# Performance work log

Measured on AMD Instinct MI355X. Metric: run time of the kernel, lower is better.

Reference implementation:

```python
import jax, jax.numpy as jnp
import numpy as np

NUM_HEADS = 16
THETA = 10000.0


def _apply_rope(x, pos):
    # x: [b, h, t, d_k], pos: [t] int
    d = x.shape[-1]
    inv_freq = THETA ** (-jnp.arange(0, d, 2, dtype=jnp.float32) / d)  # [d/2]
    ang = pos.astype(jnp.float32)[:, None] * inv_freq                  # [t, d/2]
    cos, sin = jnp.cos(ang), jnp.sin(ang)
    x1, x2 = x[..., ::2], x[..., 1::2]
    r1 = x1 * cos - x2 * sin
    r2 = x1 * sin + x2 * cos
    return jnp.stack([r1, r2], axis=-1).reshape(x.shape)


def setup_inputs() -> dict:
    key = jax.random.key(0)
    k1, k2, k3 = jax.random.split(key, 3)
    b, t, dm = 4, 2048, 2048
    in_features = jax.random.normal(k1, (b, t, dm), dtype=jnp.float32)
    token_positions = jnp.arange(t, dtype=jnp.int64)
    W_qkv = jax.random.normal(k2, (3 * dm, dm), dtype=jnp.float32) * 0.02
    W_o = jax.random.normal(k3, (dm, dm), dtype=jnp.float32) * 0.02
    return {"in_features": in_features, "token_positions": token_positions,
            "W_qkv": W_qkv, "W_o": W_o}


def reference(in_features, token_positions, W_qkv, W_o):
    b, t, dm = in_features.shape
    h = NUM_HEADS
    dk = dm // h
    # fused QKV projection (Linear: y = x W^T)
    qkv = in_features @ W_qkv.T                       # [b, t, 3*dm]
    q, k, v = jnp.split(qkv, 3, axis=-1)
    def to_heads(x):
        return x.reshape(b, t, h, dk).transpose(0, 2, 1, 3)  # [b, h, t, dk]
    q, k, v = to_heads(q), to_heads(k), to_heads(v)
    q = _apply_rope(q, token_positions)
    k = _apply_rope(k, token_positions)
    # causal SDPA
    scale = 1.0 / np.sqrt(dk).astype(np.float32)
    scores = jnp.einsum('bhqd,bhkd->bhqk', q, k) * scale
    causal = jnp.tril(jnp.ones((t, t), dtype=bool))
    scores = jnp.where(causal, scores, jnp.finfo(scores.dtype).min)
    attn = jax.nn.softmax(scores, axis=-1)
    out = jnp.einsum('bhqk,bhkd->bhqd', attn, v)      # [b, h, t, dk]
    out = out.transpose(0, 2, 1, 3).reshape(b, t, dm)
    return out @ W_o.T
```

## Files before the change

kernel.cpp:

```cpp
#include <hip/hip_runtime.h>

typedef unsigned short u16;
typedef __attribute__((ext_vector_type(8))) short s8v;
typedef __attribute__((ext_vector_type(8))) __bf16 bf8;
typedef __attribute__((ext_vector_type(4))) float f4v;

#define GLB(p) ((const __attribute__((address_space(1))) void*)(p))
#define LDS(p) ((__attribute__((address_space(3))) void*)(p))

static __device__ __forceinline__ float b2f(u16 u) {
    union { unsigned int i; float f; } v; v.i = ((unsigned int)u) << 16; return v.f;
}
static __device__ __forceinline__ u16 f2b(float f) {
    union { float f; unsigned int i; } v; v.f = f;
    v.i += 0x7fffu + ((v.i >> 16) & 1u);
    return (u16)(v.i >> 16);
}

__global__ __launch_bounds__(256) void k_conv(const float* __restrict__ in,
                                              u16* __restrict__ out, int n4) {
    int i = blockIdx.x * 256 + threadIdx.x;
    if (i >= n4) return;
    float4 v = ((const float4*)in)[i];
    union { u16 u[4]; unsigned long long ll; } o;
    o.u[0] = f2b(v.x); o.u[1] = f2b(v.y); o.u[2] = f2b(v.z); o.u[3] = f2b(v.w);
    ((unsigned long long*)out)[i] = o.ll;
}

template<int MODE>
__global__ __launch_bounds__(512, 2) void k_gemm_bt(
    const u16* __restrict__ A, const u16* __restrict__ B,
    int K, int N, int gx,
    u16* __restrict__ Qb, u16* __restrict__ Kb, u16* __restrict__ Vt,
    float* __restrict__ Cf)
{
    extern __shared__ __align__(16) u16 Ls[];

    const int t    = threadIdx.x;
    const int lane = t & 63;
    const int wid  = t >> 6;
    const int wm = wid >> 2, wn = wid & 3;
    const int la = lane & 15, lb = lane >> 4;

    const int bid = (int)blockIdx.x;
    const int id2 = (bid & 7) * ((int)gridDim.x >> 3) + (bid >> 3);
    const int bx = id2 % gx, by = id2 / gx;
    const long arow0 = (long)by * 256;
    const long brow0 = (long)bx * 256;

    const int sr = t >> 3;
    const int sg = (t & 7) ^ (sr & 7);
    const u16* Asrc = A + (arow0 + sr) * (long)K + sg * 8;
    const u16* Bsrc = B + (brow0 + sr) * (long)K + sg * 8;
    const long K64 = 64 * (long)K, K128 = 128 * (long)K;
    u16* ldst = Ls + t * 8;

#define STG(q_, op_, h_, kt_) do {                                              \
        const u16* s_ = ((op_) ? Bsrc : Asrc) + (h_) * K128 + (long)(kt_) * 64; \
        u16* d_ = ldst + (q_) * 32768 + (op_) * 16384 + (h_) * 8192;            \
        __builtin_amdgcn_global_load_lds(GLB(s_),       LDS(d_),        16, 0, 0); \
        __builtin_amdgcn_global_load_lds(GLB(s_ + K64), LDS(d_ + 4096), 16, 0, 0); \
    } while (0)
#define RD(off) (*(const bf8*)(Ls + (off)))

    f4v acc[8][4];
#pragma unroll
    for (int m = 0; m < 8; m++)
#pragma unroll
        for (int n = 0; n < 4; n++) acc[m][n] = (f4v){0.f, 0.f, 0.f, 0.f};

    const int r7 = la & 7;
    const int gA0 = (lb ^ r7) * 8;
    const int gA1 = ((lb ^ r7) ^ 4) * 8;
    const int aRow = wm * 8192 + la * 64;
    const int bRow = 16384 + (wn >> 1) * 8192 + ((wn & 1) * 64 + la) * 64;

    const int NKT = K >> 6;
    STG(0, 0, 0, 0); STG(0, 0, 1, 0); STG(0, 1, 0, 0); STG(0, 1, 1, 0);
    asm volatile("s_waitcnt vmcnt(0)" ::: "memory");
    __builtin_amdgcn_s_barrier();

    for (int X = 0; X < NKT; ++X) {
        const int D = (X & 1) << 15;
        const int q = (X + 1) & 1;
        const int S = (X + 1 < NKT) ? X + 1 : NKT - 1;
        bf8 aR[4][2], b0[2][2], b1[2][2];

#pragma unroll
        for (int mi = 0; mi < 4; mi++) {
            aR[mi][0] = RD(D + aRow + mi * 1024 + gA0);
            aR[mi][1] = RD(D + aRow + mi * 1024 + gA1);
        }
#pragma unroll
        for (int nl = 0; nl < 2; nl++) {
            b0[nl][0] = RD(D + bRow + nl * 1024 + gA0);
            b0[nl][1] = RD(D + bRow + nl * 1024 + gA1);
        }
        STG(q, 0, 0, S); STG(q, 0, 1, S); STG(q, 1, 0, S); STG(q, 1, 1, S);
        __builtin_amdgcn_s_barrier();
        __builtin_amdgcn_s_setprio(1);
#pragma unroll
        for (int mi = 0; mi < 4; mi++)
#pragma unroll
            for (int nl = 0; nl < 2; nl++) {
                acc[mi][nl] = __builtin_amdgcn_mfma_f32_16x16x32_bf16(aR[mi][0], b0[nl][0], acc[mi][nl], 0, 0, 0);
                acc[mi][nl] = __builtin_amdgcn_mfma_f32_16x16x32_bf16(aR[mi][1], b0[nl][1], acc[mi][nl], 0, 0, 0);
            }
        __builtin_amdgcn_s_setprio(0);

#pragma unroll
        for (int nl = 0; nl < 2; nl++) {
            b1[nl][0] = RD(D + bRow + (2 + nl) * 1024 + gA0);
            b1[nl][1] = RD(D + bRow + (2 + nl) * 1024 + gA1);
        }
        __builtin_amdgcn_s_barrier();
        __builtin_amdgcn_s_setprio(1);
#pragma unroll
        for (int mi = 0; mi < 4; mi++)
#pragma unroll
            for (int nl = 0; nl < 2; nl++) {
                acc[mi][2 + nl] = __builtin_amdgcn_mfma_f32_16x16x32_bf16(aR[mi][0], b1[nl][0], acc[mi][2 + nl], 0, 0, 0);
                acc[mi][2 + nl] = __builtin_amdgcn_mfma_f32_16x16x32_bf16(aR[mi][1], b1[nl][1], acc[mi][2 + nl], 0, 0, 0);
            }
        __builtin_amdgcn_s_setprio(0);

#pragma unroll
        for (int mi = 0; mi < 4; mi++) {
            aR[mi][0] = RD(D + aRow + (4 + mi) * 1024 + gA0);
            aR[mi][1] = RD(D + aRow + (4 + mi) * 1024 + gA1);
        }
        __builtin_amdgcn_s_barrier();
        __builtin_amdgcn_s_setprio(1);
#pragma unroll
        for (int mi = 0; mi < 4; mi++)
#pragma unroll
            for (int nl = 0; nl < 2; nl++) {
                acc[4 + mi][2 + nl] = __builtin_amdgcn_mfma_f32_16x16x32_bf16(aR[mi][0], b1[nl][0], acc[4 + mi][2 + nl], 0, 0, 0);
                acc[4 + mi][2 + nl] = __builtin_amdgcn_mfma_f32_16x16x32_bf16(aR[mi][1], b1[nl][1], acc[4 + mi][2 + nl], 0, 0, 0);
            }
        __builtin_amdgcn_s_setprio(0);

        asm volatile("s_waitcnt vmcnt(0)" ::: "memory");
        __builtin_amdgcn_s_barrier();
        __builtin_amdgcn_s_setprio(1);
#pragma unroll
        for (int mi = 0; mi < 4; mi++)
#pragma unroll
            for (int nl = 0; nl < 2; nl++) {
                acc[4 + mi][nl] = __builtin_amdgcn_mfma_f32_16x16x32_bf16(aR[mi][0], b0[nl][0], acc[4 + mi][nl], 0, 0, 0);
                acc[4 + mi][nl] = __builtin_amdgcn_mfma_f32_16x16x32_bf16(aR[mi][1], b0[nl][1], acc[4 + mi][nl], 0, 0, 0);
            }
        __builtin_amdgcn_s_setprio(0);
    }
#undef STG
#undef RD

    if (MODE == 1) {
#pragma unroll
        for (int mi = 0; mi < 8; mi++)
#pragma unroll
            for (int ni = 0; ni < 4; ni++) {
                const long grow0 = arow0 + wm * 128 + mi * 16 + lb * 4;
                const int  gcol  = (int)brow0 + wn * 64 + ni * 16 + la;
#pragma unroll
                for (int i = 0; i < 4; i++)
                    Cf[(grow0 + i) * (long)N + gcol] = acc[mi][ni][i];
            }
        return;
    }

    __syncthreads();
    const int part = (int)(brow0 >> 11);
    const int colp = (int)brow0 & 2047;
    const int h0   = colp >> 7;
    const int bidx = (int)(arow0 >> 11);
    const int t0   = (int)arow0 & 2047;

    if (part == 2) {
#pragma unroll
        for (int mi = 0; mi < 8; mi++)
#pragma unroll
            for (int ni = 0; ni < 4; ni++) {
                const int tlb = wm * 128 + mi * 16 + lb * 4;
                const int dl  = wn * 64 + ni * 16 + la;
#pragma unroll
                for (int i2 = 0; i2 < 2; i2++) {
                    unsigned int pk = (unsigned int)f2b(acc[mi][ni][i2 * 2])
                                    | ((unsigned int)f2b(acc[mi][ni][i2 * 2 + 1]) << 16);
                    *(unsigned int*)(Ls + dl * 264 + tlb + i2 * 2) = pk;
                }
            }
        __syncthreads();
        const int w = wid;
#pragma unroll
        for (int j = 0; j < 16; j++) {
            const int dl = j * 16 + w * 2 + (lane >> 5);
            const int c  = lane & 31;
            bf8 v = *(const bf8*)(Ls + dl * 264 + c * 8);
            const long bh = (long)(bidx * 16 + h0 + (dl >> 7));
            *(bf8*)(Vt + (bh << 18) + ((long)(dl & 127) << 11) + t0 + c * 8) = v;
        }
    } else {
        u16* dst = (part == 0) ? Qb : Kb;
#pragma unroll
        for (int mi = 0; mi < 8; mi++)
#pragma unroll
            for (int ni = 0; ni < 4; ni++) {
                const int tlb = wm * 128 + mi * 16 + lb * 4;
                const int dl  = wn * 64 + ni * 16 + la;
#pragma unroll
                for (int i = 0; i < 4; i++)
                    Ls[(tlb + i) * 264 + dl] = f2b(acc[mi][ni][i]);
            }
        __syncthreads();
#pragma unroll
        for (int j = 0; j < 16; j++) {
            const int R  = j * 32 + (t >> 4);
            const int tl = R >> 1, hh = R & 1, c = t & 15;
            bf8 v = *(const bf8*)(Ls + tl * 264 + hh * 128 + c * 8);
            const long bh = (long)(bidx * 16 + h0 + hh);
            *(bf8*)(dst + ((bh << 11) + t0 + tl) * 128 + c * 8) = v;
        }
    }
}

__global__ __launch_bounds__(256) void k_rope(u16* __restrict__ Qb, u16* __restrict__ Kb,
                                              const int* __restrict__ pos) {
    const int idx = blockIdx.x * 256 + threadIdx.x;
    const int j  = idx & 63;
    const int t  = (idx >> 6) & 2047;
    const int bh = (idx >> 17) & 63;
    u16* P = (idx >> 23) ? Kb : Qb;
    const long off = ((((long)bh << 11) + t) << 7) + 2 * j;
    unsigned int raw = *(unsigned int*)(P + off);
    float x1 = b2f((u16)(raw & 0xffffu));
    float x2 = b2f((u16)(raw >> 16));
    float invf = exp2f((float)j * -0.20762050593046014f);
    float ang = (float)pos[t] * invf;
    float sn, cs;
    sincosf(ang, &sn, &cs);
    unsigned int o = (unsigned int)f2b(x1 * cs - x2 * sn)
                   | ((unsigned int)f2b(x1 * sn + x2 * cs) << 16);
    *(unsigned int*)(P + off) = o;
}

__global__ __launch_bounds__(512) void k_attn(const u16* __restrict__ Qb,
                                              const u16* __restrict__ Kb,
                                              const u16* __restrict__ Vt,
                                              u16* __restrict__ Ob)
{
    __shared__ __align__(16) u16 Ks[2][32 * 128];
    __shared__ __align__(16) u16 Vs[2][64 * 64];
    __shared__ __align__(16) u16 Pl[8][32 * 32];

    const int tid  = threadIdx.x;
    const int lane = tid & 63;
    const int w    = tid >> 6;
    const int la = lane & 15, lb = lane >> 4;
    const int qg = 7 - ((int)blockIdx.x >> 6);
    const int bh = blockIdx.x & 63;
    const long base = (long)bh << 18;
    const int qt = qg * 8 + w;
    const int q0 = qt * 32;
    const int tiles_w = qt + 1;
    const int NT = qg * 8 + 8;
    const float scale = 0.08838834764831845f;

    bf8 qf[2][4];
#pragma unroll
    for (int m = 0; m < 2; m++)
#pragma unroll
        for (int kb = 0; kb < 4; kb++)
            qf[m][kb] = *(const bf8*)(Qb + base + (long)(q0 + m * 16 + la) * 128 + kb * 32 + lb * 8);

    f4v o[2][8];
#pragma unroll
    for (int m = 0; m < 2; m++)
#pragma unroll
        for (int n = 0; n < 8; n++) o[m][n] = (f4v){0.f, 0.f, 0.f, 0.f};
    float lst[2][4];
#pragma unroll
    for (int m = 0; m < 2; m++)
#pragma unroll
        for (int i = 0; i < 4; i++) lst[m][i] = 0.f;

    char* Pb = (char*)(Pl[w]);

    const int ko = tid * 16;
    const int kr = ko >> 8, kc = (ko & 255) ^ ((kr & 7) << 4);
    const int vo = tid * 16;
    const int vR = vo >> 7, vc = (vo & 127) ^ ((vR & 7) << 4);
    const int vd = 2 * vR + (vc >> 6), vt = (vc & 63) >> 1;

#define STAGE(buf, jt_) do {                                                        \
        const int kv0_ = (jt_) * 32;                                               \
        __builtin_amdgcn_global_load_lds(                                          \
            GLB(Kb + base + (long)(kv0_ + kr) * 128 + (kc >> 1)),                  \
            LDS((u16*)Ks[buf] + tid * 8), 16, 0, 0);                               \
        __builtin_amdgcn_global_load_lds(                                          \
            GLB(Vt + base + ((long)vd << 11) + kv0_ + vt),                         \
            LDS((u16*)Vs[buf] + tid * 8), 16, 0, 0);                               \
    } while (0)

    STAGE(0, 0);

    for (int jt = 0; jt < NT; ++jt) {
        const int buf = jt & 1;
        __syncthreads();
        if (jt + 1 < NT) STAGE(buf ^ 1, jt + 1);

        if (jt < tiles_w) {
            const char* KsB = (const char*)Ks[buf];
            const char* VsB = (const char*)Vs[buf];

            f4v s[2][2];
            s[0][0] = s[0][1] = s[1][0] = s[1][1] = (f4v){0.f, 0.f, 0.f, 0.f};
#pragma unroll
            for (int n = 0; n < 2; n++) {
                const int row = n * 16 + la;
#pragma unroll
                for (int kb = 0; kb < 4; kb++) {
                    bf8 kf = *(const bf8*)(KsB + row * 256 + ((kb * 64 + lb * 16) ^ ((row & 7) << 4)));
                    s[0][n] = __builtin_amdgcn_mfma_f32_16x16x32_bf16(qf[0][kb], kf, s[0][n], 0, 0, 0);
                    s[1][n] = __builtin_amdgcn_mfma_f32_16x16x32_bf16(qf[1][kb], kf, s[1][n], 0, 0, 0);
                }
            }

            bf8 vf[8];
#pragma unroll
            for (int nO = 0; nO < 8; nO++) {
                const int R = nO * 8 + (la >> 1);
                vf[nO] = *(const bf8*)(VsB + R * 128 + (((la & 1) * 64 + lb * 16) ^ ((R & 7) << 4)));
            }

            const bool diag = (jt == qt);
            float p[2][2][4];
#pragma unroll
            for (int m = 0; m < 2; m++)
#pragma unroll
                for (int n = 0; n < 2; n++)
#pragma unroll
                    for (int i = 0; i < 4; i++) {
                        float v = __expf(fmaf(s[m][n][i], scale, -8.0f));
                        if (diag && (n * 16 + la) > (m * 16 + lb * 4 + i)) v = 0.f;
                        p[m][n][i] = v;
                        lst[m][i] += v;
                    }

#pragma unroll
            for (int m = 0; m < 2; m++)
#pragma unroll
                for (int n = 0; n < 2; n++)
#pragma unroll
                    for (int i = 0; i < 4; i++) {
                        const int row = m * 16 + lb * 4 + i;
                        const int colb = (n * 16 + la) * 2;
                        *(u16*)(Pb + row * 64 + (colb ^ ((row & 3) << 4))) = f2b(p[m][n][i]);
                    }
            bf8 pa[2];
#pragma unroll
            for (int am = 0; am < 2; am++) {
                const int row = am * 16 + la;
                pa[am] = *(const bf8*)(Pb + row * 64 + ((lb * 16) ^ ((row & 3) << 4)));
            }
#pragma unroll
            for (int nO = 0; nO < 8; nO++) {
                o[0][nO] = __builtin_amdgcn_mfma_f32_16x16x32_bf16(pa[0], vf[nO], o[0][nO], 0, 0, 0);
                o[1][nO] = __builtin_amdgcn_mfma_f32_16x16x32_bf16(pa[1], vf[nO], o[1][nO], 0, 0, 0);
            }
        }
        __syncthreads();
    }
#undef STAGE

    float linv[2][4];
#pragma unroll
    for (int m = 0; m < 2; m++)
#pragma unroll
        for (int i = 0; i < 4; i++) {
            float l = lst[m][i];
            l += __shfl_xor(l, 1);
            l += __shfl_xor(l, 2);
            l += __shfl_xor(l, 4);
            l += __shfl_xor(l, 8);
            linv[m][i] = 1.0f / l;
        }

    const int b = bh >> 4, h = bh & 15;
#pragma unroll
    for (int m = 0; m < 2; m++)
#pragma unroll
        for (int nO = 0; nO < 8; nO++)
#pragma unroll
            for (int i = 0; i < 4; i++) {
                const int row = q0 + m * 16 + lb * 4 + i;
                const int d = nO * 16 + la;
                Ob[((long)(b * 2048 + row) << 11) + h * 128 + d] = f2b(o[m][nO][i] * linv[m][i]);
            }
}

extern "C" void kernel_launch(void* const* d_in, const int* in_sizes, int n_in,
                              void* d_out, int out_size, void* d_ws, size_t ws_size,
                              hipStream_t stream)
{
    const float* X    = (const float*)d_in[0];
    const int*   pos  = (const int*)d_in[1];
    const float* Wqkv = (const float*)d_in[2];
    const float* Wo   = (const float*)d_in[3];
    float* out = (float*)d_out;

    char* ws = (char*)d_ws;
    u16* Xb    = (u16*)(ws + 0);
    u16* Wqkvb = (u16*)(ws + 33554432);
    u16* Wob   = (u16*)(ws + 58720256);
    u16* Qb    = (u16*)(ws + 67108864);
    u16* Kb    = (u16*)(ws + 100663296);
    u16* Vt    = (u16*)(ws + 134217728);
    u16* Ob    = (u16*)(ws + 167772160);

    k_conv<<<16384, 256, 0, stream>>>(X, Xb, 4194304);
    k_conv<<<12288, 256, 0, stream>>>(Wqkv, Wqkvb, 3145728);
    k_conv<<<4096, 256, 0, stream>>>(Wo, Wob, 1048576);
    k_gemm_bt<0><<<768, 512, 139392, stream>>>(Xb, Wqkvb, 2048, 6144, 24, Qb, Kb, Vt, nullptr);
    k_rope<<<65536, 256, 0, stream>>>(Qb, Kb, pos);
    k_attn<<<512, 512, 0, stream>>>(Qb, Kb, Vt, Ob);
    k_gemm_bt<1><<<256, 512, 139392, stream>>>(Ob, Wob, 2048, 2048, 8, nullptr, nullptr, nullptr, out);
}
```

Before: 436.2 us.

## Fuse RoPE into QKV GEMM epilogue, merge conversions, triple-buffer GEMM k-loop

Three separate changes. The three fp32-to-bf16 conversion launches become one launch that picks its source by index. RoPE moves into the Q/K store epilogue of the QKV GEMM, using fast __sincosf, so the standalone rope pass that re-read and re-wrote Q and K is gone. The GEMM main loop switches from a 64-wide double-buffered k-tile with four barriers per step to a 32-wide triple-buffered tile with one barrier per step, keeping more loads in flight. The risks are lower sincos accuracy at large angles and a different LDS bank pattern from the new 4-way swizzle.

```diff
diff --git a/kernel.cpp b/kernel.cpp
--- a/kernel.cpp
+++ b/kernel.cpp
@@ -17,14 +17,21 @@
     return (u16)(v.i >> 16);
 }
 
-__global__ __launch_bounds__(256) void k_conv(const float* __restrict__ in,
-                                              u16* __restrict__ out, int n4) {
+__global__ __launch_bounds__(256) void k_conv(const float* __restrict__ X,
+                                              const float* __restrict__ Wq,
+                                              const float* __restrict__ Wo,
+                                              u16* __restrict__ Xb,
+                                              u16* __restrict__ Wqb,
+                                              u16* __restrict__ Wob) {
     int i = blockIdx.x * 256 + threadIdx.x;
-    if (i >= n4) return;
-    float4 v = ((const float4*)in)[i];
+    const float* in; u16* out; int off;
+    if (i < 4194304)      { in = X;  out = Xb;  off = i; }
+    else if (i < 7340032) { in = Wq; out = Wqb; off = i - 4194304; }
+    else                  { in = Wo; out = Wob; off = i - 7340032; }
+    float4 v = ((const float4*)in)[off];
     union { u16 u[4]; unsigned long long ll; } o;
     o.u[0] = f2b(v.x); o.u[1] = f2b(v.y); o.u[2] = f2b(v.z); o.u[3] = f2b(v.w);
-    ((unsigned long long*)out)[i] = o.ll;
+    ((unsigned long long*)out)[off] = o.ll;
 }
 
 template<int MODE>
@@ -32,7 +39,7 @@
     const u16* __restrict__ A, const u16* __restrict__ B,
     int K, int N, int gx,
     u16* __restrict__ Qb, u16* __restrict__ Kb, u16* __restrict__ Vt,
-    float* __restrict__ Cf)
+    float* __restrict__ Cf, const int* __restrict__ pos)
 {
     extern __shared__ __align__(16) u16 Ls[];
 
@@ -48,18 +55,20 @@
     const long arow0 = (long)by * 256;
     const long brow0 = (long)bx * 256;
 
-    const int sr = t >> 3;
-    const int sg = (t & 7) ^ (sr & 7);
+    const int sr = t >> 2;
+    const int sg = (t & 3) ^ (sr & 3);
     const u16* Asrc = A + (arow0 + sr) * (long)K + sg * 8;
     const u16* Bsrc = B + (brow0 + sr) * (long)K + sg * 8;
-    const long K64 = 64 * (long)K, K128 = 128 * (long)K;
+    const long K128 = 128 * (long)K;
     u16* ldst = Ls + t * 8;
 
-#define STG(q_, op_, h_, kt_) do {                                              \
-        const u16* s_ = ((op_) ? Bsrc : Asrc) + (h_) * K128 + (long)(kt_) * 64; \
-        u16* d_ = ldst + (q_) * 32768 + (op_) * 16384 + (h_) * 8192;            \
-        __builtin_amdgcn_global_load_lds(GLB(s_),       LDS(d_),        16, 0, 0); \
-        __builtin_amdgcn_global_load_lds(GLB(s_ + K64), LDS(d_ + 4096), 16, 0, 0); \
+#define STG(q_, kt_) do {                                                          \
+        const long ko_ = (long)(kt_) * 32;                                         \
+        u16* d_ = ldst + (q_) * 16384;                                             \
+        __builtin_amdgcn_global_load_lds(GLB(Asrc + ko_),         LDS(d_),         16, 0, 0); \
+        __builtin_amdgcn_global_load_lds(GLB(Asrc + K128 + ko_),  LDS(d_ + 4096),  16, 0, 0); \
+        __builtin_amdgcn_global_load_lds(GLB(Bsrc + ko_),         LDS(d_ + 8192),  16, 0, 0); \
+        __builtin_amdgcn_global_load_lds(GLB(Bsrc + K128 + ko_),  LDS(d_ + 12288), 16, 0, 0); \
     } while (0)
 #define RD(off) (*(const bf8*)(Ls + (off)))
 
@@ -69,89 +78,38 @@
 #pragma unroll
         for (int n = 0; n < 4; n++) acc[m][n] = (f4v){0.f, 0.f, 0.f, 0.f};
 
-    const int r7 = la & 7;
-    const int gA0 = (lb ^ r7) * 8;
-    const int gA1 = ((lb ^ r7) ^ 4) * 8;
-    const int aRow = wm * 8192 + la * 64;
-    const int bRow = 16384 + (wn >> 1) * 8192 + ((wn & 1) * 64 + la) * 64;
-
-    const int NKT = K >> 6;
-    STG(0, 0, 0, 0); STG(0, 0, 1, 0); STG(0, 1, 0, 0); STG(0, 1, 1, 0);
+    const int gA = (lb ^ (la & 3)) * 8;
+    const int aBase = wm * 4096 + la * 32 + gA;
+    const int bBase = 8192 + (wn >> 1) * 4096 + ((wn & 1) * 64 + la) * 32 + gA;
+
+    const int NKT = K >> 5;
+    STG(0, 0); STG(1, 1);
+    asm volatile("s_waitcnt vmcnt(4)" ::: "memory");
+    __builtin_amdgcn_s_barrier();
+
+    for (int X = 0; X < NKT; ++X) {
+        const int D = (X % 3) * 16384;
+        int S = X + 2; if (S > NKT - 1) S = NKT - 1;
+        STG((X + 2) % 3, S);
+
+        bf8 aF[8], bF[4];
+#pragma unroll
+        for (int mi = 0; mi < 8; mi++) aF[mi] = RD(D + aBase + mi * 512);
+#pragma unroll
+        for (int ni = 0; ni < 4; ni++) bF[ni] = RD(D + bBase + ni * 512);
+
+        __builtin_amdgcn_s_setprio(1);
+#pragma unroll
+        for (int mi = 0; mi < 8; mi++)
+#pragma unroll
+            for (int ni = 0; ni < 4; ni++)
+                acc[mi][ni] = __builtin_amdgcn_mfma_f32_16x16x32_bf16(aF[mi], bF[ni], acc[mi][ni], 0, 0, 0);
+        __builtin_amdgcn_s_setprio(0);
+
+        asm volatile("s_waitcnt vmcnt(4)" ::: "memory");
+        __builtin_amdgcn_s_barrier();
+    }
     asm volatile("s_waitcnt vmcnt(0)" ::: "memory");
-    __builtin_amdgcn_s_barrier();
-
-    for (int X = 0; X < NKT; ++X) {
-        const int D = (X & 1) << 15;
-        const int q = (X + 1) & 1;
-        const int S = (X + 1 < NKT) ? X + 1 : NKT - 1;
-        bf8 aR[4][2], b0[2][2], b1[2][2];
-
-#pragma unroll
-        for (int mi = 0; mi < 4; mi++) {
-            aR[mi][0] = RD(D + aRow + mi * 1024 + gA0);
-            aR[mi][1] = RD(D + aRow + mi * 1024 + gA1);
-        }
-#pragma unroll
-        for (int nl = 0; nl < 2; nl++) {
-            b0[nl][0] = RD(D + bRow + nl * 1024 + gA0);
-            b0[nl][1] = RD(D + bRow + nl * 1024 + gA1);
-        }
-        STG(q, 0, 0, S); STG(q, 0, 1, S); STG(q, 1, 0, S); STG(q, 1, 1, S);
-        __builtin_amdgcn_s_barrier();
-        __builtin_amdgcn_s_setprio(1);
-#pragma unroll
-        for (int mi = 0; mi < 4; mi++)
-#pragma unroll
-            for (int nl = 0; nl < 2; nl++) {
-                acc[mi][nl] = __builtin_amdgcn_mfma_f32_16x16x32_bf16(aR[mi][0], b0[nl][0], acc[mi][nl], 0, 0, 0);
-                acc[mi][nl] = __builtin_amdgcn_mfma_f32_16x16x32_bf16(aR[mi][1], b0[nl][1], acc[mi][nl], 0, 0, 0);
-            }
-        __builtin_amdgcn_s_setprio(0);
-
-#pragma unroll
-        for (int nl = 0; nl < 2; nl++) {
-            b1[nl][0] = RD(D + bRow + (2 + nl) * 1024 + gA0);
-            b1[nl][1] = RD(D + bRow + (2 + nl) * 1024 + gA1);
-        }
-        __builtin_amdgcn_s_barrier();
-        __builtin_amdgcn_s_setprio(1);
-#pragma unroll
-        for (int mi = 0; mi < 4; mi++)
-#pragma unroll
-            for (int nl = 0; nl < 2; nl++) {
-                acc[mi][2 + nl] = __builtin_amdgcn_mfma_f32_16x16x32_bf16(aR[mi][0], b1[nl][0], acc[mi][2 + nl], 0, 0, 0);
-                acc[mi][2 + nl] = __builtin_amdgcn_mfma_f32_16x16x32_bf16(aR[mi][1], b1[nl][1], acc[mi][2 + nl], 0, 0, 0);
-            }
-        __builtin_amdgcn_s_setprio(0);
-
-#pragma unroll
-        for (int mi = 0; mi < 4; mi++) {
-            aR[mi][0] = RD(D + aRow + (4 + mi) * 1024 + gA0);
-            aR[mi][1] = RD(D + aRow + (4 + mi) * 1024 + gA1);
-        }
-        __builtin_amdgcn_s_barrier();
-        __builtin_amdgcn_s_setprio(1);
-#pragma unroll
-        for (int mi = 0; mi < 4; mi++)
-#pragma unroll
-            for (int nl = 0; nl < 2; nl++) {
-                acc[4 + mi][2 + nl] = __builtin_amdgcn_mfma_f32_16x16x32_bf16(aR[mi][0], b1[nl][0], acc[4 + mi][2 + nl], 0, 0, 0);
-                acc[4 + mi][2 + nl] = __builtin_amdgcn_mfma_f32_16x16x32_bf16(aR[mi][1], b1[nl][1], acc[4 + mi][2 + nl], 0, 0, 0);
-            }
-        __builtin_amdgcn_s_setprio(0);
-
-        asm volatile("s_waitcnt vmcnt(0)" ::: "memory");
-        __builtin_amdgcn_s_barrier();
-        __builtin_amdgcn_s_setprio(1);
-#pragma unroll
-        for (int mi = 0; mi < 4; mi++)
-#pragma unroll
-            for (int nl = 0; nl < 2; nl++) {
-                acc[4 + mi][nl] = __builtin_amdgcn_mfma_f32_16x16x32_bf16(aR[mi][0], b0[nl][0], acc[4 + mi][nl], 0, 0, 0);
-                acc[4 + mi][nl] = __builtin_amdgcn_mfma_f32_16x16x32_bf16(aR[mi][1], b0[nl][1], acc[4 + mi][nl], 0, 0, 0);
-            }
-        __builtin_amdgcn_s_setprio(0);
-    }
 #undef STG
 #undef RD
 
@@ -191,10 +149,9 @@
                 }
             }
         __syncthreads();
-        const int w = wid;
 #pragma unroll
         for (int j = 0; j < 16; j++) {
-            const int dl = j * 16 + w * 2 + (lane >> 5);
+            const int dl = j * 16 + wid * 2 + (lane >> 5);
             const int c  = lane & 31;
             bf8 v = *(const bf8*)(Ls + dl * 264 + c * 8);
             const long bh = (long)(bidx * 16 + h0 + (dl >> 7));
@@ -213,35 +170,31 @@
                     Ls[(tlb + i) * 264 + dl] = f2b(acc[mi][ni][i]);
             }
         __syncthreads();
+        const int c = t & 15;
+        float invf[4];
+#pragma unroll
+        for (int p2 = 0; p2 < 4; p2++)
+            invf[p2] = exp2f((float)(c * 4 + p2) * -0.20762050593046014f);
 #pragma unroll
         for (int j = 0; j < 16; j++) {
             const int R  = j * 32 + (t >> 4);
-            const int tl = R >> 1, hh = R & 1, c = t & 15;
-            bf8 v = *(const bf8*)(Ls + tl * 264 + hh * 128 + c * 8);
+            const int tl = R >> 1, hh = R & 1;
+            s8v v = *(const s8v*)(Ls + tl * 264 + hh * 128 + c * 8);
+            const float pf = (float)pos[t0 + tl];
+            union { u16 u[8]; s8v v; } ov;
+#pragma unroll
+            for (int p2 = 0; p2 < 4; p2++) {
+                float x1 = b2f((u16)v[2 * p2]);
+                float x2 = b2f((u16)v[2 * p2 + 1]);
+                float sn, cs;
+                __sincosf(pf * invf[p2], &sn, &cs);
+                ov.u[2 * p2]     = f2b(x1 * cs - x2 * sn);
+                ov.u[2 * p2 + 1] = f2b(x1 * sn + x2 * cs);
+            }
             const long bh = (long)(bidx * 16 + h0 + hh);
-            *(bf8*)(dst + ((bh << 11) + t0 + tl) * 128 + c * 8) = v;
+            *(s8v*)(dst + ((bh << 11) + t0 + tl) * 128 + c * 8) = ov.v;
         }
     }
-}
-
-__global__ __launch_bounds__(256) void k_rope(u16* __restrict__ Qb, u16* __restrict__ Kb,
-                                              const int* __restrict__ pos) {
-    const int idx = blockIdx.x * 256 + threadIdx.x;
-    const int j  = idx & 63;
-    const int t  = (idx >> 6) & 2047;
-    const int bh = (idx >> 17) & 63;
-    u16* P = (idx >> 23) ? Kb : Qb;
-    const long off = ((((long)bh << 11) + t) << 7) + 2 * j;
-    unsigned int raw = *(unsigned int*)(P + off);
-    float x1 = b2f((u16)(raw & 0xffffu));
-    float x2 = b2f((u16)(raw >> 16));
-    float invf = exp2f((float)j * -0.20762050593046014f);
-    float ang = (float)pos[t] * invf;
-    float sn, cs;
-    sincosf(ang, &sn, &cs);
-    unsigned int o = (unsigned int)f2b(x1 * cs - x2 * sn)
-                   | ((unsigned int)f2b(x1 * sn + x2 * cs) << 16);
-    *(unsigned int*)(P + off) = o;
 }
 
 __global__ __launch_bounds__(512) void k_attn(const u16* __restrict__ Qb,
@@ -418,11 +371,8 @@
     u16* Vt    = (u16*)(ws + 134217728);
     u16* Ob    = (u16*)(ws + 167772160);
 
-    k_conv<<<16384, 256, 0, stream>>>(X, Xb, 4194304);
-    k_conv<<<12288, 256, 0, stream>>>(Wqkv, Wqkvb, 3145728);
-    k_conv<<<4096, 256, 0, stream>>>(Wo, Wob, 1048576);
-    k_gemm_bt<0><<<768, 512, 139392, stream>>>(Xb, Wqkvb, 2048, 6144, 24, Qb, Kb, Vt, nullptr);
-    k_rope<<<65536, 256, 0, stream>>>(Qb, Kb, pos);
+    k_conv<<<32768, 256, 0, stream>>>(X, Wqkv, Wo, Xb, Wqkvb, Wob);
+    k_gemm_bt<0><<<768, 512, 135168, stream>>>(Xb, Wqkvb, 2048, 6144, 24, Qb, Kb, Vt, nullptr, pos);
     k_attn<<<512, 512, 0, stream>>>(Qb, Kb, Vt, Ob);
-    k_gemm_bt<1><<<256, 512, 139392, stream>>>(Ob, Wob, 2048, 2048, 8, nullptr, nullptr, nullptr, out);
-}
+    k_gemm_bt<1><<<256, 512, 98304, stream>>>(Ob, Wob, 2048, 2048, 8, nullptr, nullptr, nullptr, out, nullptr);
+}
```

Result: slower. 455.0 us (+4.3%).
